# Kernel tuning notes

Measured on AMD Instinct MI355X. Metric: run time of the kernel, lower is better.

## Reference

```python
import jax, jax.numpy as jnp
import numpy as np

N_LAYERS = 5
EMB = 300
G = 2048
L_SEM = 10
V_SEM = 30
NUM_TASKS = 128
TAU = 1.0
GUM_TAU = 1.0
BN_EPS = 1e-5


def _bn(x, g, b):
    # training-mode batch norm (biased variance over batch dim)
    m = jnp.mean(x, 0)
    v = jnp.var(x, 0)
    return (x - m) / jnp.sqrt(v + BN_EPS) * g + b


def setup_inputs() -> dict:
    key = jax.random.key(0)
    ks = iter(jax.random.split(key, 64))
    N, E = 100000, 400000
    s = 0.02
    inp = {}
    inp['x_idx'] = jax.random.randint(next(ks), (N,), 0, 119)
    inp['edge_index'] = jax.random.randint(next(ks), (2, E), 0, N)
    inp['edge_attr'] = jax.random.randint(next(ks), (E,), 0, 5)
    inp['batch'] = jnp.sort(jax.random.randint(next(ks), (N,), 0, G))
    u = jax.random.uniform(next(ks), (G, L_SEM, V_SEM), minval=1e-8, maxval=1.0)
    inp['gumbel'] = -jnp.log(-jnp.log(u))  # standard Gumbel(0,1) noise
    nrm = lambda shape: jax.random.normal(next(ks), shape, dtype=jnp.float32) * s
    inp['atom_emb'] = nrm((119, EMB))
    inp['bond_emb'] = nrm((N_LAYERS, 5, EMB))
    inp['eps'] = jnp.zeros((N_LAYERS,), jnp.float32)
    inp['gin_W1'] = nrm((N_LAYERS, EMB, 2 * EMB)); inp['gin_b1'] = jnp.zeros((N_LAYERS, 2 * EMB))
    inp['gin_bn1_g'] = jnp.ones((N_LAYERS, 2 * EMB)); inp['gin_bn1_b'] = jnp.zeros((N_LAYERS, 2 * EMB))
    inp['gin_W2'] = nrm((N_LAYERS, 2 * EMB, EMB)); inp['gin_b2'] = jnp.zeros((N_LAYERS, EMB))
    inp['node_bn_g'] = jnp.ones((N_LAYERS, EMB)); inp['node_bn_b'] = jnp.zeros((N_LAYERS, EMB))
    M = N_LAYERS - 1
    inp['vn_W1'] = nrm((M, EMB, 2 * EMB)); inp['vn_b1'] = jnp.zeros((M, 2 * EMB))
    inp['vn_bn1_g'] = jnp.ones((M, 2 * EMB)); inp['vn_bn1_b'] = jnp.zeros((M, 2 * EMB))
    inp['vn_W2'] = nrm((M, 2 * EMB, EMB)); inp['vn_b2'] = jnp.zeros((M, EMB))
    inp['vn_bn2_g'] = jnp.ones((M, EMB)); inp['vn_bn2_b'] = jnp.zeros((M, EMB))
    inp['pre_W'] = nrm((EMB, L_SEM * V_SEM)); inp['pre_b'] = jnp.zeros((L_SEM * V_SEM,))
    inp['sel_W'] = nrm((V_SEM, 3)); inp['sel_b'] = jnp.zeros((3,))
    inp['aft_W'] = nrm((3 * L_SEM, EMB)); inp['aft_b'] = jnp.zeros((EMB,))
    inp['hW1'] = nrm((EMB, 128)); inp['hb1'] = jnp.zeros((128,))
    inp['hW2'] = nrm((128, 128)); inp['hb2'] = jnp.zeros((128,))
    inp['hW3'] = nrm((128, NUM_TASKS)); inp['hb3'] = jnp.zeros((NUM_TASKS,))
    return inp


def reference(x_idx, edge_index, edge_attr, batch, gumbel,
              atom_emb, bond_emb, eps,
              gin_W1, gin_b1, gin_bn1_g, gin_bn1_b, gin_W2, gin_b2,
              node_bn_g, node_bn_b,
              vn_W1, vn_b1, vn_bn1_g, vn_bn1_b, vn_W2, vn_b2, vn_bn2_g, vn_bn2_b,
              pre_W, pre_b, sel_W, sel_b, aft_W, aft_b,
              hW1, hb1, hW2, hb2, hW3, hb3):
    N = x_idx.shape[0]
    src, dst = edge_index[0], edge_index[1]
    h = atom_emb[x_idx]                               # [N, EMB]
    vn = jnp.zeros((G, EMB), h.dtype)                 # virtual node starts at zero embedding
    for l in range(N_LAYERS):
        hl = h + vn[batch]
        # GINConv: aggregate relu(x_src + bond_emb) onto dst, then MLP((1+eps)x + aggr)
        msg = jax.nn.relu(hl[src] + bond_emb[l][edge_attr])   # [E, EMB]
        agg = jax.ops.segment_sum(msg, dst, num_segments=N)
        t = (1.0 + eps[l]) * hl + agg
        t = jax.nn.relu(_bn(t @ gin_W1[l] + gin_b1[l], gin_bn1_g[l], gin_bn1_b[l]))
        t = t @ gin_W2[l] + gin_b2[l]
        t = _bn(t, node_bn_g[l], node_bn_b[l])
        if l < N_LAYERS - 1:
            t = jax.nn.relu(t)
            # virtual node update (dropout omitted: eval mode)
            vtmp = jax.ops.segment_sum(hl, batch, num_segments=G) + vn
            v1 = jax.nn.relu(_bn(vtmp @ vn_W1[l] + vn_b1[l], vn_bn1_g[l], vn_bn1_b[l]))
            vn = jax.nn.relu(_bn(v1 @ vn_W2[l] + vn_b2[l], vn_bn2_g[l], vn_bn2_b[l]))
        h = t
    # global mean pool
    cnt = jnp.maximum(jax.ops.segment_sum(jnp.ones((N,), h.dtype), batch, num_segments=G), 1.0)
    h_graph = jax.ops.segment_sum(h, batch, num_segments=G) / cnt[:, None]
    # SEM head: gumbel-softmax (hard, straight-through)
    logits = ((h_graph @ pre_W + pre_b) / TAU).reshape(G, L_SEM, V_SEM)
    y = (logits + gumbel) / GUM_TAU
    y_soft = jax.nn.softmax(y, axis=-1)
    y_hard = jax.nn.one_hot(jnp.argmax(y, axis=-1), V_SEM, dtype=y_soft.dtype)
    oht = jax.lax.stop_gradient(y_hard - y_soft) + y_soft
    msg_w = oht @ sel_W + sel_b                        # [G, L, 3]
    dis = msg_w.reshape(G, 3 * L_SEM) @ aft_W + aft_b  # [G, EMB]
    o = jax.nn.relu(dis @ hW1 + hb1)
    o = jax.nn.relu(o @ hW2 + hb2)
    return o @ hW3 + hb3                               # [G, num_tasks]
```

## Files before the change

### kernel.cpp

```cpp
#include <hip/hip_runtime.h>
#include <cstdint>

#define EMBD 300
#define GNUM 2048
#define LSEM 10
#define VSEM 30
#define NLAY 5
#define GRAM_KB 24

typedef __attribute__((ext_vector_type(8))) short short8v;
typedef __attribute__((ext_vector_type(4))) float f32x4;

__device__ __forceinline__ void split3(float x, short& h1, short& h2, short& h3) {
  unsigned u = __float_as_uint(x);
  unsigned uh = (u + 0x7FFFu + ((u >> 16) & 1u)) & 0xFFFF0000u;
  h1 = (short)(uh >> 16);
  float r = x - __uint_as_float(uh);
  unsigned v = __float_as_uint(r);
  unsigned vh = (v + 0x7FFFu + ((v >> 16) & 1u)) & 0xFFFF0000u;
  h2 = (short)(vh >> 16);
  float r2 = r - __uint_as_float(vh);
  unsigned w = __float_as_uint(r2);
  unsigned wh = (w + 0x7FFFu + ((w >> 16) & 1u)) & 0xFFFF0000u;
  h3 = (short)(wh >> 16);
}

__device__ __forceinline__ unsigned cvt_pk_bf16(float lo, float hi) {
  unsigned r;
  asm("v_cvt_pk_bf16_f32 %0, %1, %2" : "=v"(r) : "v"(lo), "v"(hi));
  return r;
}

__device__ __forceinline__ void split3_pair(float x0, float x1,
                                            unsigned& u1, unsigned& u2, unsigned& u3) {
  u1 = cvt_pk_bf16(x0, x1);
  float r0 = x0 - __uint_as_float(u1 << 16);
  float r1 = x1 - __uint_as_float(u1 & 0xFFFF0000u);
  u2 = cvt_pk_bf16(r0, r1);
  float s0 = r0 - __uint_as_float(u2 << 16);
  float s1 = r1 - __uint_as_float(u2 & 0xFFFF0000u);
  u3 = cvt_pk_bf16(s0, s1);
}

__global__ void k_diag(float* __restrict__ p, int n, float v) {
  int i = blockIdx.x * blockDim.x + threadIdx.x;
  if (i < n) p[i] = v;
}

__global__ void k_zero(float* __restrict__ p, int n) {
  int i = blockIdx.x * blockDim.x + threadIdx.x;
  if (i < n) p[i] = 0.f;
}

__global__ void k_seti(int* __restrict__ p, int n, int v) {
  int i = blockIdx.x * blockDim.x + threadIdx.x;
  if (i < n) p[i] = v;
}

__global__ void k_offsets(const int* __restrict__ batch, int N, int* __restrict__ off) {
  int g = blockIdx.x * blockDim.x + threadIdx.x;
  if (g > GNUM) return;
  int lo = 0, hi = N;
  while (lo < hi) { int mid = (lo + hi) >> 1; if (batch[mid] < g) lo = mid + 1; else hi = mid; }
  off[g] = lo;
}

__global__ void k_deg(const int* __restrict__ dst, int E, int* __restrict__ deg) {
  int e = blockIdx.x * blockDim.x + threadIdx.x;
  if (e < E) atomicAdd(&deg[dst[e]], 1);
}

__global__ void k_scan1(const int* __restrict__ deg, int N,
                        int* __restrict__ incl, int* __restrict__ part) {
  __shared__ int s[256];
  int tid = threadIdx.x;
  int i = blockIdx.x * 256 + tid;
  int v = (i < N) ? deg[i] : 0;
  s[tid] = v; __syncthreads();
  for (int o = 1; o < 256; o <<= 1) {
    int t = (tid >= o) ? s[tid - o] : 0;
    __syncthreads();
    s[tid] += t;
    __syncthreads();
  }
  if (i < N) incl[i] = s[tid];
  if (tid == 255) part[blockIdx.x] = s[255];
}

__global__ void k_scan2(int* __restrict__ part, int nb) {
  __shared__ int s[512];
  int t = threadIdx.x;
  if (nb <= 512) {
    int v = (t < nb) ? part[t] : 0;
    s[t] = v; __syncthreads();
    for (int o = 1; o < 512; o <<= 1) {
      int u = (t >= o) ? s[t - o] : 0;
      __syncthreads();
      s[t] += u;
      __syncthreads();
    }
    if (t < nb) part[t] = s[t] - v;
  } else if (t == 0) {
    int run = 0;
    for (int i = 0; i < nb; i++) { int x = part[i]; part[i] = run; run += x; }
  }
}

__global__ void k_scan3(const int* __restrict__ deg, const int* __restrict__ incl,
                        const int* __restrict__ part, int N, int E, int* __restrict__ off2) {
  int i = blockIdx.x * blockDim.x + threadIdx.x;
  if (i < N) off2[i] = part[i >> 8] + incl[i] - deg[i];
  if (i == 0) off2[N] = E;
}

__global__ void k_copyi(const int* __restrict__ a, int* __restrict__ b, int n) {
  int i = blockIdx.x * blockDim.x + threadIdx.x;
  if (i < n) b[i] = a[i];
}

__global__ void k_fill(const int* __restrict__ dst, int E,
                       int* __restrict__ cur, int* __restrict__ eix) {
  int e = blockIdx.x * blockDim.x + threadIdx.x;
  if (e >= E) return;
  int p = atomicAdd(&cur[dst[e]], 1);
  eix[p] = e;
}

template<bool FIRST>
__global__ void k_hl(const float* __restrict__ aemb, const int* __restrict__ x_idx,
                     const float* __restrict__ scale, const float* __restrict__ shift,
                     const int* __restrict__ batch, const float* __restrict__ vn,
                     const float* __restrict__ epsArr, int l,
                     float* pt, float* __restrict__ hl, int N)
{
  int i = blockIdx.x;
  int c = threadIdx.x;
  if (c >= EMBD) return;
  float x;
  if (FIRST) {
    x = aemb[(size_t)x_idx[i] * EMBD + c];
  } else {
    x = pt[(size_t)i * EMBD + c];
    x = fmaxf(fmaf(x, scale[c], shift[c]), 0.f);
  }
  float h = x + vn[(size_t)batch[i] * EMBD + c];
  hl[(size_t)i * EMBD + c] = h;
  pt[(size_t)i * EMBD + c] = (1.f + epsArr[l]) * h;
}

__global__ void k_gather(const int* __restrict__ off2, const int* __restrict__ eix,
                         const int* __restrict__ src, const int* __restrict__ eattr,
                         const float* __restrict__ hl, const float* __restrict__ bond,
                         float* __restrict__ tacc, int N)
{
  int node = blockIdx.x * 4 + (threadIdx.x >> 6);
  int lane = threadIdx.x & 63;
  if (node >= N) return;
  int p0 = off2[node], p1 = off2[node + 1];
  if (p0 == p1) return;
  float acc[5] = {0.f, 0.f, 0.f, 0.f, 0.f};
  for (int p = p0; p < p1; p++) {
    int e = eix[p];
    int s = src[e], a = eattr[e];
    const float* hr = hl + (size_t)s * EMBD;
    const float* br = bond + (size_t)a * EMBD;
    #pragma unroll
    for (int q = 0; q < 5; q++) {
      int c = lane + q * 64;
      if (c < EMBD) {
        float v = hr[c] + br[c];
        acc[q] += fmaxf(v, 0.f);
      }
    }
  }
  float* tr = tacc + (size_t)node * EMBD;
  #pragma unroll
  for (int q = 0; q < 5; q++) {
    int c = lane + q * 64;
    if (c < EMBD) tr[c] += acc[q];
  }
}

__global__ void k_splitW(const float* __restrict__ W, int K, int Kpad, int M,
                         short* __restrict__ planes)
{
  int idx = blockIdx.x * 256 + threadIdx.x;
  if (idx >= M * Kpad) return;
  int m = idx / Kpad, k = idx - m * Kpad;
  float x = (k < K) ? W[(size_t)k * M + m] : 0.f;
  short h1, h2, h3; split3(x, h1, h2, h3);
  size_t ps = (size_t)M * Kpad;
  planes[idx] = h1; planes[ps + idx] = h2; planes[2 * ps + idx] = h3;
}

template<int CT, bool AFUSE>
__global__ __launch_bounds__(256) void k_mgemm(
    const float* __restrict__ A, const short* __restrict__ Wp,
    const float* __restrict__ bias, float* __restrict__ C,
    int n, int K, int Kpad, int M,
    const float* __restrict__ ascale, const float* __restrict__ ashift)
{
  __shared__ __align__(16) short lsA[3][64][40];
  __shared__ __align__(16) short lsB[3][CT * 64][40];
  int tid = threadIdx.x;
  int row0 = blockIdx.x * 64;
  int col0 = blockIdx.y * (CT * 64);
  int l = tid & 63, wid = tid >> 6;
  int wr = wid >> 1, wc = wid & 1;
  int lr = l & 15, kb = (l >> 4) * 8, rbase = (l >> 4) * 4;
  int sar = tid >> 2;
  int sak = (tid & 3) * 8;
  size_t planeSz = (size_t)M * Kpad;

  f32x4 acc[2][CT * 2];
  #pragma unroll
  for (int i = 0; i < 2; i++)
    #pragma unroll
    for (int j = 0; j < CT * 2; j++) acc[i][j] = (f32x4){0.f, 0.f, 0.f, 0.f};

  for (int k0 = 0; k0 < Kpad; k0 += 32) {
    {
      int gr = row0 + sar;
      int kbase = k0 + sak;
      float x[8];
      if (gr < n && kbase + 7 < K) {
        const float* ap = A + (size_t)gr * K + kbase;
        float4 u0 = *reinterpret_cast<const float4*>(ap);
        float4 u1 = *reinterpret_cast<const float4*>(ap + 4);
        x[0] = u0.x; x[1] = u0.y; x[2] = u0.z; x[3] = u0.w;
        x[4] = u1.x; x[5] = u1.y; x[6] = u1.z; x[7] = u1.w;
        if (AFUSE) {
          float4 sc0 = *reinterpret_cast<const float4*>(ascale + kbase);
          float4 sc1 = *reinterpret_cast<const float4*>(ascale + kbase + 4);
          float4 sf0 = *reinterpret_cast<const float4*>(ashift + kbase);
          float4 sf1 = *reinterpret_cast<const float4*>(ashift + kbase + 4);
          x[0] = fmaxf(fmaf(x[0], sc0.x, sf0.x), 0.f);
          x[1] = fmaxf(fmaf(x[1], sc0.y, sf0.y), 0.f);
          x[2] = fmaxf(fmaf(x[2], sc0.z, sf0.z), 0.f);
          x[3] = fmaxf(fmaf(x[3], sc0.w, sf0.w), 0.f);
          x[4] = fmaxf(fmaf(x[4], sc1.x, sf1.x), 0.f);
          x[5] = fmaxf(fmaf(x[5], sc1.y, sf1.y), 0.f);
          x[6] = fmaxf(fmaf(x[6], sc1.z, sf1.z), 0.f);
          x[7] = fmaxf(fmaf(x[7], sc1.w, sf1.w), 0.f);
        }
      } else {
        #pragma unroll
        for (int j = 0; j < 8; j++) {
          int k = kbase + j;
          float v = 0.f;
          if (gr < n && k < K) {
            v = A[(size_t)gr * K + k];
            if (AFUSE) v = fmaxf(fmaf(v, ascale[k], ashift[k]), 0.f);
          }
          x[j] = v;
        }
      }
      uint4 q1, q2, q3;
      unsigned* p1 = (unsigned*)&q1; unsigned* p2 = (unsigned*)&q2; unsigned* p3 = (unsigned*)&q3;
      #pragma unroll
      for (int j = 0; j < 4; j++) split3_pair(x[2 * j], x[2 * j + 1], p1[j], p2[j], p3[j]);
      *reinterpret_cast<uint4*>(&lsA[0][sar][sak]) = q1;
      *reinterpret_cast<uint4*>(&lsA[1][sar][sak]) = q2;
      *reinterpret_cast<uint4*>(&lsA[2][sar][sak]) = q3;
    }
    if constexpr (CT == 2) {
      int sbc = tid >> 1;
      int sbk = (tid & 1) * 16;
      int gc = col0 + sbc;
      #pragma unroll
      for (int p = 0; p < 3; p++) {
        short8v v0, v1;
        if (gc < M) {
          const short* bp = Wp + (size_t)p * planeSz + (size_t)gc * Kpad + k0 + sbk;
          v0 = *reinterpret_cast<const short8v*>(bp);
          v1 = *reinterpret_cast<const short8v*>(bp + 8);
        } else {
          #pragma unroll
          for (int j = 0; j < 8; j++) { v0[j] = 0; v1[j] = 0; }
        }
        *reinterpret_cast<short8v*>(&lsB[p][sbc][sbk]) = v0;
        *reinterpret_cast<short8v*>(&lsB[p][sbc][sbk + 8]) = v1;
      }
    } else {
      int sbc = tid >> 2;
      int sbk = (tid & 3) * 8;
      int gc = col0 + sbc;
      #pragma unroll
      for (int p = 0; p < 3; p++) {
        short8v v0;
        if (gc < M) {
          const short* bp = Wp + (size_t)p * planeSz + (size_t)gc * Kpad + k0 + sbk;
          v0 = *reinterpret_cast<const short8v*>(bp);
        } else {
          #pragma unroll
          for (int j = 0; j < 8; j++) v0[j] = 0;
        }
        *reinterpret_cast<short8v*>(&lsB[p][sbc][sbk]) = v0;
      }
    }
    __syncthreads();
    short8v fa[3][2];
    #pragma unroll
    for (int p = 0; p < 3; p++)
      #pragma unroll
      for (int rf = 0; rf < 2; rf++)
        fa[p][rf] = *reinterpret_cast<const short8v*>(&lsA[p][wr * 32 + rf * 16 + lr][kb]);
    #pragma unroll
    for (int cf = 0; cf < CT * 2; cf++) {
      int bcol = wc * (CT * 32) + cf * 16 + lr;
      short8v fb0 = *reinterpret_cast<const short8v*>(&lsB[0][bcol][kb]);
      short8v fb1 = *reinterpret_cast<const short8v*>(&lsB[1][bcol][kb]);
      short8v fb2 = *reinterpret_cast<const short8v*>(&lsB[2][bcol][kb]);
      #pragma unroll
      for (int rf = 0; rf < 2; rf++) {
        f32x4 a = acc[rf][cf];
        a = __builtin_amdgcn_mfma_f32_16x16x32_bf16(fa[0][rf], fb0, a, 0, 0, 0);
        a = __builtin_amdgcn_mfma_f32_16x16x32_bf16(fa[0][rf], fb1, a, 0, 0, 0);
        a = __builtin_amdgcn_mfma_f32_16x16x32_bf16(fa[1][rf], fb0, a, 0, 0, 0);
        a = __builtin_amdgcn_mfma_f32_16x16x32_bf16(fa[1][rf], fb1, a, 0, 0, 0);
        a = __builtin_amdgcn_mfma_f32_16x16x32_bf16(fa[0][rf], fb2, a, 0, 0, 0);
        a = __builtin_amdgcn_mfma_f32_16x16x32_bf16(fa[2][rf], fb0, a, 0, 0, 0);
        acc[rf][cf] = a;
      }
    }
    __syncthreads();
  }
  #pragma unroll
  for (int rf = 0; rf < 2; rf++) {
    #pragma unroll
    for (int cf = 0; cf < CT * 2; cf++) {
      int col = col0 + wc * (CT * 32) + cf * 16 + lr;
      if (col >= M) continue;
      float bv = bias[col];
      #pragma unroll
      for (int r = 0; r < 4; r++) {
        int row = row0 + wr * 32 + rf * 16 + rbase + r;
        if (row < n) C[(size_t)row * M + col] = acc[rf][cf][r] + bv;
      }
    }
  }
}

template<bool AFUSE, bool ORELU>
__global__ __launch_bounds__(256) void k_gemm(
    const float* __restrict__ A, const float* __restrict__ W,
    const float* __restrict__ bias, float* __restrict__ C,
    int N, int K, int M,
    const float* __restrict__ ascale, const float* __restrict__ ashift)
{
  __shared__ __align__(16) float As[16][72];
  __shared__ __align__(16) float Bs[16][72];
  int tid = threadIdx.x;
  int row0 = blockIdx.x * 64;
  int col0 = blockIdx.y * 64;
  int tx = tid & 15, ty = tid >> 4;
  bool kvec = ((K & 3) == 0);
  bool mvec = ((M & 3) == 0);
  float acc[4][4] = {};
  for (int k0 = 0; k0 < K; k0 += 16) {
    {
      int r = tid >> 2;
      int kq = (tid & 3) * 4;
      int gr = row0 + r;
      float a0 = 0.f, a1 = 0.f, a2 = 0.f, a3 = 0.f;
      if (gr < N) {
        const float* ap = A + (size_t)gr * K + k0 + kq;
        int k = k0 + kq;
        if (kvec && k + 3 < K) {
          float4 t = *reinterpret_cast<const float4*>(ap);
          a0 = t.x; a1 = t.y; a2 = t.z; a3 = t.w;
        } else {
          if (k + 0 < K) a0 = ap[0];
          if (k + 1 < K) a1 = ap[1];
          if (k + 2 < K) a2 = ap[2];
          if (k + 3 < K) a3 = ap[3];
        }
        if (AFUSE) {
          if (k + 0 < K) a0 = fmaxf(fmaf(a0, ascale[k + 0], ashift[k + 0]), 0.f);
          if (k + 1 < K) a1 = fmaxf(fmaf(a1, ascale[k + 1], ashift[k + 1]), 0.f);
          if (k + 2 < K) a2 = fmaxf(fmaf(a2, ascale[k + 2], ashift[k + 2]), 0.f);
          if (k + 3 < K) a3 = fmaxf(fmaf(a3, ascale[k + 3], ashift[k + 3]), 0.f);
        }
      }
      As[kq + 0][r] = a0; As[kq + 1][r] = a1; As[kq + 2][r] = a2; As[kq + 3][r] = a3;
    }
    {
      int kk = tid >> 4;
      int j = (tid & 15) * 4;
      int gk = k0 + kk;
      float4 bv = {0.f, 0.f, 0.f, 0.f};
      if (gk < K) {
        const float* wp = W + (size_t)gk * M + col0 + j;
        if (mvec && col0 + j + 3 < M) {
          bv = *reinterpret_cast<const float4*>(wp);
        } else {
          if (col0 + j + 0 < M) bv.x = wp[0];
          if (col0 + j + 1 < M) bv.y = wp[1];
          if (col0 + j + 2 < M) bv.z = wp[2];
          if (col0 + j + 3 < M) bv.w = wp[3];
        }
      }
      *reinterpret_cast<float4*>(&Bs[kk][j]) = bv;
    }
    __syncthreads();
    #pragma unroll
    for (int kk = 0; kk < 16; kk++) {
      float4 a4 = *reinterpret_cast<const float4*>(&As[kk][ty * 4]);
      float4 b4 = *reinterpret_cast<const float4*>(&Bs[kk][tx * 4]);
      float a[4] = {a4.x, a4.y, a4.z, a4.w};
      float b[4] = {b4.x, b4.y, b4.z, b4.w};
      #pragma unroll
      for (int u = 0; u < 4; u++)
        #pragma unroll
        for (int v = 0; v < 4; v++)
          acc[u][v] = fmaf(a[u], b[v], acc[u][v]);
    }
    __syncthreads();
  }
  float bv[4];
  #pragma unroll
  for (int v = 0; v < 4; v++) { int gc = col0 + tx * 4 + v; bv[v] = (gc < M) ? bias[gc] : 0.f; }
  #pragma unroll
  for (int u = 0; u < 4; u++) {
    int gr = row0 + ty * 4 + u;
    if (gr >= N) continue;
    int gc0 = col0 + tx * 4;
    float val[4];
    #pragma unroll
    for (int v = 0; v < 4; v++) {
      float x = acc[u][v] + bv[v];
      if (ORELU) x = fmaxf(x, 0.f);
      val[v] = x;
    }
    if (mvec && gc0 + 3 < M) {
      float4 o = {val[0], val[1], val[2], val[3]};
      *reinterpret_cast<float4*>(C + (size_t)gr * M + gc0) = o;
    } else {
      #pragma unroll
      for (int v = 0; v < 4; v++) {
        int gc = gc0 + v;
        if (gc < M) C[(size_t)gr * M + gc] = val[v];
      }
    }
  }
}

__global__ __launch_bounds__(256) void k_gram(const float* __restrict__ A, int N,
                                              double* __restrict__ gpart)
{
  int bx = blockIdx.x;
  int ti = 0;
  {
    const int o1 = 5, o2 = 9, o3 = 12, o4 = 14;
    if (bx >= o1) ti = 1;
    if (bx >= o2) ti = 2;
    if (bx >= o3) ti = 3;
    if (bx >= o4) ti = 4;
  }
  const int offs[5] = {0, 5, 9, 12, 14};
  int tj = ti + (bx - offs[ti]);
  int I = ti * 64, J = tj * 64;
  __shared__ __align__(16) float LI[128][68];
  __shared__ __align__(16) float LJ[128][68];
  int tid = threadIdx.x;
  int tx = tid & 15, ty = tid >> 4;
  double dacc[4][4] = {};
  for (int rb = blockIdx.y; rb * 128 < N; rb += gridDim.y) {
    int r0 = rb * 128;
    {
      int rbase = tid >> 4;
      int c4 = (tid & 15) * 4;
      #pragma unroll
      for (int s = 0; s < 8; s++) {
        int r = rbase + s * 16;
        int gr = r0 + r;
        float4 vi = {0.f, 0.f, 0.f, 0.f}, vj = {0.f, 0.f, 0.f, 0.f};
        if (gr < N) {
          int ci = I + c4;
          if (ci + 3 < EMBD) vi = *reinterpret_cast<const float4*>(A + (size_t)gr * EMBD + ci);
          int cj = J + c4;
          if (cj + 3 < EMBD) vj = *reinterpret_cast<const float4*>(A + (size_t)gr * EMBD + cj);
        }
        *reinterpret_cast<float4*>(&LI[r][c4]) = vi;
        *reinterpret_cast<float4*>(&LJ[r][c4]) = vj;
      }
    }
    __syncthreads();
    float facc[4][4] = {};
    #pragma unroll 2
    for (int k = 0; k < 128; k++) {
      float4 a4 = *reinterpret_cast<const float4*>(&LI[k][ty * 4]);
      float4 b4 = *reinterpret_cast<const float4*>(&LJ[k][tx * 4]);
      float a[4] = {a4.x, a4.y, a4.z, a4.w};
      float b[4] = {b4.x, b4.y, b4.z, b4.w};
      #pragma unroll
      for (int u = 0; u < 4; u++)
        #pragma unroll
        for (int v = 0; v < 4; v++)
          facc[u][v] = fmaf(a[u], b[v], facc[u][v]);
    }
    #pragma unroll
    for (int u = 0; u < 4; u++)
      #pragma unroll
      for (int v = 0; v < 4; v++)
        dacc[u][v] += (double)facc[u][v];
    __syncthreads();
  }
  size_t base = ((size_t)blockIdx.y * 15 + bx) * 4096;
  #pragma unroll
  for (int u = 0; u < 4; u++)
    #pragma unroll
    for (int v = 0; v < 4; v++)
      gpart[base + (size_t)(ty * 4 + u) * 64 + tx * 4 + v] = dacc[u][v];
}

__global__ void k_gramfin(const double* __restrict__ gpart, double* __restrict__ G)
{
  int e = blockIdx.x * 256 + threadIdx.x;
  if (e >= 15 * 4096) return;
  int tile = e >> 12;
  int ii = (e >> 6) & 63, jj = e & 63;
  const int tit[15] = {0,0,0,0,0,1,1,1,1,2,2,2,3,3,4};
  const int tjt[15] = {0,1,2,3,4,1,2,3,4,2,3,4,3,4,4};
  int gi = tit[tile] * 64 + ii, gj = tjt[tile] * 64 + jj;
  if (gi >= EMBD || gj >= EMBD) return;
  double s = 0.0;
  for (int kb = 0; kb < GRAM_KB; kb++)
    s += gpart[((size_t)kb * 15 + tile) * 4096 + ii * 64 + jj];
  G[(size_t)gi * EMBD + gj] = s;
  G[(size_t)gj * EMBD + gi] = s;
}

__global__ void k_bn1gram(const double* __restrict__ G, const double* __restrict__ cbuf,
                          const float* __restrict__ W1, const float* __restrict__ b1,
                          const float* __restrict__ g, const float* __restrict__ b,
                          int n, float* __restrict__ sc, float* __restrict__ sh)
{
  int j = blockIdx.x;
  int t = threadIdx.x;
  __shared__ double ws[EMBD];
  __shared__ double red[256];
  for (int k = t; k < EMBD; k += 256) ws[k] = (double)W1[(size_t)k * 600 + j];
  __syncthreads();
  int i1 = 256 + t;
  double y0 = 0.0, y1 = 0.0;
  for (int k = 0; k < EMBD; k++) {
    double wk = ws[k];
    y0 += G[(size_t)k * EMBD + t] * wk;
    if (i1 < EMBD) y1 += G[(size_t)k * EMBD + i1] * wk;
  }
  double part = ws[t] * y0 + ((i1 < EMBD) ? ws[i1] * y1 : 0.0);
  double dpart = cbuf[t] * ws[t] + ((i1 < EMBD) ? cbuf[i1] * ws[i1] : 0.0);
  red[t] = part; __syncthreads();
  for (int w = 128; w > 0; w >>= 1) { if (t < w) red[t] += red[t + w]; __syncthreads(); }
  double Q = red[0]; __syncthreads();
  red[t] = dpart; __syncthreads();
  for (int w = 128; w > 0; w >>= 1) { if (t < w) red[t] += red[t + w]; __syncthreads(); }
  if (t == 0) {
    double d = red[0];
    double bj = (double)b1[j];
    double S = d + (double)n * bj;
    double Qf = Q + 2.0 * bj * d + (double)n * bj * bj;
    double m = S / n;
    double var = Qf / n - m * m;
    double inv = 1.0 / sqrt(var + 1e-5);
    double scv = (double)g[j] * inv;
    sc[j] = (float)scv;
    sh[j] = (float)((double)b[j] - m * scv);
  }
}

__global__ void k_colstats(const float* __restrict__ X, int n, int C,
                           double* __restrict__ psum, double* __restrict__ psq)
{
  int tid = threadIdx.x;
  int col = blockIdx.x * 64 + (tid & 63);
  int rl = tid >> 6;
  double s = 0.0, q = 0.0;
  if (col < C) {
    int stride = gridDim.y * 4;
    for (int r = blockIdx.y * 4 + rl; r < n; r += stride) {
      double x = (double)X[(size_t)r * C + col];
      s += x; q += x * x;
    }
  }
  __shared__ double ls[2][4][64];
  ls[0][rl][tid & 63] = s;
  ls[1][rl][tid & 63] = q;
  __syncthreads();
  if (rl == 0 && col < C) {
    int c = tid & 63;
    double S = ls[0][0][c] + ls[0][1][c] + ls[0][2][c] + ls[0][3][c];
    double Q = ls[1][0][c] + ls[1][1][c] + ls[1][2][c] + ls[1][3][c];
    psum[(size_t)blockIdx.y * C + col] = S;
    psq [(size_t)blockIdx.y * C + col] = Q;
  }
}

__global__ void k_redcol(const double* __restrict__ psum, int R, int C, double* __restrict__ cbuf)
{
  int c = blockIdx.x * blockDim.x + threadIdx.x;
  if (c >= C) return;
  double s = 0.0;
  for (int r = 0; r < R; r++) s += psum[(size_t)r * C + c];
  cbuf[c] = s;
}

__global__ void k_finstats(const double* __restrict__ psum, const double* __restrict__ psq,
                           int R, int M, int n,
                           const float* __restrict__ g, const float* __restrict__ b,
                           float* __restrict__ sc, float* __restrict__ sh)
{
  int j = blockIdx.x;
  int t = threadIdx.x;
  double s = 0.0, q = 0.0;
  for (int r = t; r < R; r += 256) { s += psum[(size_t)r * M + j]; q += psq[(size_t)r * M + j]; }
  __shared__ double ls[256], lq[256];
  ls[t] = s; lq[t] = q; __syncthreads();
  for (int w = 128; w > 0; w >>= 1) {
    if (t < w) { ls[t] += ls[t + w]; lq[t] += lq[t + w]; }
    __syncthreads();
  }
  if (t == 0) {
    double m = ls[0] / n;
    double v = lq[0] / n - m * m;
    double inv = 1.0 / sqrt(v + 1e-5);
    double scv = (double)g[j] * inv;
    sc[j] = (float)scv;
    sh[j] = (float)((double)b[j] - m * scv);
  }
}

__global__ void k_vnseg(const float* __restrict__ hl, const int* __restrict__ off,
                        const float* __restrict__ vn, float* __restrict__ vtmp)
{
  int g = blockIdx.x;
  int c = threadIdx.x;
  if (c >= EMBD) return;
  int r0 = off[g], r1 = off[g + 1];
  float s = 0.f;
  for (int r = r0; r < r1; r++) s += hl[(size_t)r * EMBD + c];
  vtmp[(size_t)g * EMBD + c] = s + vn[(size_t)g * EMBD + c];
}

__global__ void k_vnfinal(const float* __restrict__ vnraw, const float* __restrict__ scale,
                          const float* __restrict__ shift, float* __restrict__ vn, int total)
{
  int i = blockIdx.x * blockDim.x + threadIdx.x;
  if (i >= total) return;
  int c = i % EMBD;
  vn[i] = fmaxf(fmaf(vnraw[i], scale[c], shift[c]), 0.f);
}

__global__ void k_pool(const float* __restrict__ t2, const int* __restrict__ off,
                       const float* __restrict__ scale, const float* __restrict__ shift,
                       float* __restrict__ hg)
{
  int g = blockIdx.x;
  int c = threadIdx.x;
  if (c >= EMBD) return;
  int r0 = off[g], r1 = off[g + 1];
  float s = 0.f;
  for (int r = r0; r < r1; r++) s += t2[(size_t)r * EMBD + c];
  int cnt = r1 - r0;
  float denom = (cnt > 0) ? (float)cnt : 1.f;
  hg[(size_t)g * EMBD + c] = (scale[c] * s + shift[c] * (float)cnt) / denom;
}

__global__ void k_sem(const float* __restrict__ logits, const float* __restrict__ gum,
                      const float* __restrict__ selW, const float* __restrict__ selb,
                      float* __restrict__ msgw)
{
  int idx = blockIdx.x * blockDim.x + threadIdx.x;
  if (idx >= GNUM * LSEM) return;
  int g = idx / LSEM, l = idx % LSEM;
  const float* lp = logits + (size_t)g * (LSEM * VSEM) + l * VSEM;
  const float* gp = gum + (size_t)g * (LSEM * VSEM) + l * VSEM;
  float best = -1e30f; int bi = 0;
  for (int v = 0; v < VSEM; v++) {
    float y = lp[v] + gp[v];
    if (y > best) { best = y; bi = v; }
  }
  float* o = msgw + (size_t)g * (3 * LSEM) + l * 3;
  o[0] = selW[bi * 3 + 0] + selb[0];
  o[1] = selW[bi * 3 + 1] + selb[1];
  o[2] = selW[bi * 3 + 2] + selb[2];
}

template<bool AFUSE, bool ORELU>
static void gemm(const float* A, const float* W, const float* b, float* C,
                 int n, int k, int m, const float* sc, const float* sh, hipStream_t st)
{
  dim3 grid((n + 63) / 64, (m + 63) / 64);
  k_gemm<AFUSE, ORELU><<<grid, 256, 0, st>>>(A, W, b, C, n, k, m, sc, sh);
}

extern "C" void kernel_launch(void* const* d_in, const int* in_sizes, int n_in,
                              void* d_out, int out_size, void* d_ws, size_t ws_size,
                              hipStream_t stream)
{
  const int*   x_idx     = (const int*)d_in[0];
  const int*   eidx      = (const int*)d_in[1];
  const int*   eattr     = (const int*)d_in[2];
  const int*   batch     = (const int*)d_in[3];
  const float* gumbel    = (const float*)d_in[4];
  const float* atom_emb  = (const float*)d_in[5];
  const float* bond_emb  = (const float*)d_in[6];
  const float* eps       = (const float*)d_in[7];
  const float* gin_W1    = (const float*)d_in[8];
  const float* gin_b1    = (const float*)d_in[9];
  const float* gin_bn1_g = (const float*)d_in[10];
  const float* gin_bn1_b = (const float*)d_in[11];
  const float* gin_W2    = (const float*)d_in[12];
  const float* gin_b2    = (const float*)d_in[13];
  const float* node_bn_g = (const float*)d_in[14];
  const float* node_bn_b = (const float*)d_in[15];
  const float* vn_W1     = (const float*)d_in[16];
  const float* vn_b1     = (const float*)d_in[17];
  const float* vn_bn1_g  = (const float*)d_in[18];
  const float* vn_bn1_b  = (const float*)d_in[19];
  const float* vn_W2     = (const float*)d_in[20];
  const float* vn_b2     = (const float*)d_in[21];
  const float* vn_bn2_g  = (const float*)d_in[22];
  const float* vn_bn2_b  = (const float*)d_in[23];
  const float* pre_W     = (const float*)d_in[24];
  const float* pre_b     = (const float*)d_in[25];
  const float* sel_W     = (const float*)d_in[26];
  const float* sel_b     = (const float*)d_in[27];
  const float* aft_W     = (const float*)d_in[28];
  const float* aft_b     = (const float*)d_in[29];
  const float* hW1       = (const float*)d_in[30];
  const float* hb1       = (const float*)d_in[31];
  const float* hW2       = (const float*)d_in[32];
  const float* hb2       = (const float*)d_in[33];
  const float* hW3       = (const float*)d_in[34];
  const float* hb3       = (const float*)d_in[35];

  const int N = in_sizes[0];
  const int E = in_sizes[2];
  const int RB = 128;
  float* out = (float*)d_out;
  (void)n_in;

  char* ws = (char*)d_ws;
  size_t pos = 0;
  auto alloc = [&](size_t bytes) -> char* {
    char* p = ws + pos;
    pos = (pos + bytes + 255) & ~(size_t)255;
    return p;
  };
  int*    off   = (int*)   alloc((GNUM + 1) * sizeof(int));
  float*  hbuf0 = (float*) alloc((size_t)N * EMBD * 4);
  float*  hbuf1 = (float*) alloc((size_t)N * EMBD * 4);
  double* psum  = (double*)alloc((size_t)RB * 600 * 8);
  double* psq   = (double*)alloc((size_t)RB * 600 * 8);
  float*  vn    = (float*) alloc((size_t)GNUM * EMBD * 4);
  float*  vtmp  = (float*) alloc((size_t)GNUM * EMBD * 4);
  float*  vnraw = (float*) alloc((size_t)GNUM * EMBD * 4);
  double* cbuf  = (double*)alloc(EMBD * 8);
  int*    off2  = (int*)   alloc((size_t)(N + 1) * 4);
  int*    eix   = (int*)   alloc((size_t)E * 4);
  short*  wsplit1 = (short*)alloc((size_t)600 * 320 * 3 * 2);
  short*  wsplit2 = (short*)alloc((size_t)300 * 608 * 3 * 2);
  float*  s1    = (float*) alloc(600 * 4);
  float*  sh1   = (float*) alloc(600 * 4);
  float*  s2    = (float*) alloc(EMBD * 4);
  float*  sh2   = (float*) alloc(EMBD * 4);
  float*  vs1   = (float*) alloc(600 * 4);
  float*  vsh1  = (float*) alloc(600 * 4);
  float*  vs2   = (float*) alloc(EMBD * 4);
  float*  vsh2  = (float*) alloc(EMBD * 4);

  const size_t gpartBytes = (size_t)GRAM_KB * 15 * 4096 * 8;
  const size_t gBytes     = (size_t)EMBD * EMBD * 8;
  const size_t csrScratch = (size_t)N * 4 * 3 + 4096;
  const long long CH_MIN  = 2048;
  size_t slack = 1u << 20;
  size_t region_need = gpartBytes + gBytes;
  if (region_need < csrScratch) region_need = csrScratch;
  size_t t1_min = (size_t)CH_MIN * 600 * 4;
  if (region_need < t1_min) region_need = t1_min;

  if (ws_size < pos + region_need + slack) {
    float v = 1000.f + (float)(ws_size >> 20);
    k_diag<<<(out_size + 255) / 256, 256, 0, stream>>>(out, out_size, v);
    return;
  }

  size_t regionBytes = ws_size - pos - slack;
  char* region = ws + pos;
  int* deg  = (int*)region;
  int* incl = (int*)(region + (size_t)N * 4);
  int* cur  = (int*)(region + (size_t)N * 8);
  int* part = (int*)(region + (size_t)N * 12);
  double* gpart = (double*)region;
  double* G     = (double*)(region + gpartBytes);
  float*  t1buf = (float*)region;
  int CH;
  {
    long long ch = (long long)(regionBytes / (600ull * 4ull));
    if (ch > 32768) ch = 32768;
    ch &= ~63LL;
    if (ch < CH_MIN) ch = CH_MIN;
    long long npad = ((long long)N + 63) & ~63LL;
    if (ch > npad && npad >= CH_MIN) ch = npad;
    CH = (int)ch;
  }
  float* v1 = t1buf;
  float* hg     = vnraw;
  float* logits = t1buf;
  float* msgw   = t1buf + (size_t)GNUM * EMBD;
  float* dis    = vtmp;
  float* o1     = vn;
  float* o2     = vn + (size_t)GNUM * 128;

  k_zero<<<(GNUM * EMBD + 255) / 256, 256, 0, stream>>>(vn, GNUM * EMBD);
  k_offsets<<<(GNUM + 1 + 255) / 256, 256, 0, stream>>>(batch, N, off);

  const int* esrc = eidx;
  const int* edst = eidx + E;

  {
    int NB = (N + 255) / 256;
    k_seti<<<(N + 255) / 256, 256, 0, stream>>>(deg, N, 0);
    k_deg<<<(E + 255) / 256, 256, 0, stream>>>(edst, E, deg);
    k_scan1<<<NB, 256, 0, stream>>>(deg, N, incl, part);
    k_scan2<<<1, 512, 0, stream>>>(part, NB);
    k_scan3<<<(N + 255) / 256, 256, 0, stream>>>(deg, incl, part, N, E, off2);
    k_copyi<<<(N + 255) / 256, 256, 0, stream>>>(off2, cur, N);
    k_fill<<<(E + 255) / 256, 256, 0, stream>>>(edst, E, cur, eix);
  }

  float* hb[2] = {hbuf0, hbuf1};

  for (int l = 0; l < NLAY; l++) {
    float* tac = hb[l & 1];
    float* hlb = hb[(l + 1) & 1];

    if (l == 0)
      k_hl<true><<<N, 320, 0, stream>>>(atom_emb, x_idx, nullptr, nullptr, batch, vn, eps, l, tac, hlb, N);
    else
      k_hl<false><<<N, 320, 0, stream>>>(nullptr, nullptr, s2, sh2, batch, vn, eps, l, tac, hlb, N);

    k_gather<<<(N + 3) / 4, 256, 0, stream>>>(off2, eix, esrc, eattr, hlb,
                                              bond_emb + (size_t)l * 5 * EMBD, tac, N);

    if (l < NLAY - 1)
      k_vnseg<<<GNUM, 320, 0, stream>>>(hlb, off, vn, vtmp);

    k_colstats<<<dim3(5, RB), 256, 0, stream>>>(tac, N, EMBD, psum, psq);
    k_redcol<<<2, 256, 0, stream>>>(psum, RB, EMBD, cbuf);
    k_gram<<<dim3(15, GRAM_KB), 256, 0, stream>>>(tac, N, gpart);
    k_gramfin<<<240, 256, 0, stream>>>(gpart, G);
    k_bn1gram<<<600, 256, 0, stream>>>(G, cbuf, gin_W1 + (size_t)l * EMBD * 600,
                                       gin_b1 + (size_t)l * 600,
                                       gin_bn1_g + (size_t)l * 600, gin_bn1_b + (size_t)l * 600,
                                       N, s1, sh1);

    k_splitW<<<(600 * 320 + 255) / 256, 256, 0, stream>>>(gin_W1 + (size_t)l * EMBD * 600, 300, 320, 600, wsplit1);
    k_splitW<<<(300 * 608 + 255) / 256, 256, 0, stream>>>(gin_W2 + (size_t)l * 600 * EMBD, 600, 608, 300, wsplit2);

    for (int r0 = 0; r0 < N; r0 += CH) {
      int nr = (N - r0 < CH) ? (N - r0) : CH;
      dim3 g1((nr + 63) / 64, 5);
      k_mgemm<2, false><<<g1, 256, 0, stream>>>(tac + (size_t)r0 * EMBD, wsplit1,
                                                gin_b1 + (size_t)l * 600, t1buf,
                                                nr, 300, 320, 600, nullptr, nullptr);
      dim3 g2((nr + 63) / 64, 5);
      k_mgemm<1, true><<<g2, 256, 0, stream>>>(t1buf, wsplit2,
                                               gin_b2 + (size_t)l * EMBD, hlb + (size_t)r0 * EMBD,
                                               nr, 600, 608, 300, s1, sh1);
    }
    k_colstats<<<dim3(5, RB), 256, 0, stream>>>(hlb, N, EMBD, psum, psq);
    k_finstats<<<EMBD, 256, 0, stream>>>(psum, psq, RB, EMBD, N,
                                         node_bn_g + (size_t)l * EMBD, node_bn_b + (size_t)l * EMBD, s2, sh2);

    if (l < NLAY - 1) {
      gemm<false, false>(vtmp, vn_W1 + (size_t)l * EMBD * 600, vn_b1 + (size_t)l * 600, v1,
                         GNUM, EMBD, 600, nullptr, nullptr, stream);
      k_colstats<<<dim3(10, RB), 256, 0, stream>>>(v1, GNUM, 600, psum, psq);
      k_finstats<<<600, 256, 0, stream>>>(psum, psq, RB, 600, GNUM,
                                          vn_bn1_g + (size_t)l * 600, vn_bn1_b + (size_t)l * 600, vs1, vsh1);
      gemm<true, false>(v1, vn_W2 + (size_t)l * 600 * EMBD, vn_b2 + (size_t)l * EMBD, vnraw,
                        GNUM, 600, EMBD, vs1, vsh1, stream);
      k_colstats<<<dim3(5, RB), 256, 0, stream>>>(vnraw, GNUM, EMBD, psum, psq);
      k_finstats<<<EMBD, 256, 0, stream>>>(psum, psq, RB, EMBD, GNUM,
                                           vn_bn2_g + (size_t)l * EMBD, vn_bn2_b + (size_t)l * EMBD, vs2, vsh2);
      k_vnfinal<<<(GNUM * EMBD + 255) / 256, 256, 0, stream>>>(vnraw, vs2, vsh2, vn, GNUM * EMBD);
    }
  }

  float* lastH = hb[NLAY & 1];
  k_pool<<<GNUM, 320, 0, stream>>>(lastH, off, s2, sh2, hg);

  gemm<false, false>(hg, pre_W, pre_b, logits, GNUM, EMBD, LSEM * VSEM, nullptr, nullptr, stream);
  k_sem<<<(GNUM * LSEM + 255) / 256, 256, 0, stream>>>(logits, gumbel, sel_W, sel_b, msgw);
  gemm<false, false>(msgw, aft_W, aft_b, dis, GNUM, 3 * LSEM, EMBD, nullptr, nullptr, stream);
  gemm<false, true>(dis, hW1, hb1, o1, GNUM, EMBD, 128, nullptr, nullptr, stream);
  gemm<false, true>(o1, hW2, hb2, o2, GNUM, 128, 128, nullptr, nullptr, stream);
  gemm<false, false>(o2, hW3, hb3, out, GNUM, 128, 128, nullptr, nullptr, stream);
}
```

Before: 10.42 ms.

## Compute Gram matrix with split-bf16 MFMA instead of scalar FP32 FMAs

Replaces the FP32 FMA Gram kernel (used for the BN1 statistics shortcut) with an MFMA version. Each float is split into three bf16 parts and six bf16 MFMA products are accumulated to approximate FP32 precision. This moves the N×300×300 Gram work onto the matrix units, which should cut the ALU cost. In exchange, accumulation is now FP32 across all rows of a block's slice, where the old kernel flushed partials into FP64 every 128 rows, so rounding error may grow.

```diff
diff --git a/kernel.cpp b/kernel.cpp
--- a/kernel.cpp
+++ b/kernel.cpp
@@ -341,6 +341,117 @@
   }
 }
 
+__global__ __launch_bounds__(256) void k_mgram(const float* __restrict__ A, int N,
+                                               double* __restrict__ gpart)
+{
+  int bx = blockIdx.x;
+  int ti = 0;
+  {
+    const int o1 = 5, o2 = 9, o3 = 12, o4 = 14;
+    if (bx >= o1) ti = 1;
+    if (bx >= o2) ti = 2;
+    if (bx >= o3) ti = 3;
+    if (bx >= o4) ti = 4;
+  }
+  const int offs[5] = {0, 5, 9, 12, 14};
+  int tj = ti + (bx - offs[ti]);
+  int I = ti * 64, J = tj * 64;
+  __shared__ __align__(16) short lsI[3][64][40];
+  __shared__ __align__(16) short lsJ[3][64][40];
+  int tid = threadIdx.x;
+  int l = tid & 63, wid = tid >> 6;
+  int wr = wid >> 1, wc = wid & 1;
+  int lr = l & 15, kb = (l >> 4) * 8, rbase = (l >> 4) * 4;
+  int sr = tid & 31;
+  int sc0 = (tid >> 5) * 8;
+
+  f32x4 acc[2][2];
+  #pragma unroll
+  for (int i = 0; i < 2; i++)
+    #pragma unroll
+    for (int j = 0; j < 2; j++) acc[i][j] = (f32x4){0.f, 0.f, 0.f, 0.f};
+
+  for (int r0 = blockIdx.y * 32; r0 < N; r0 += gridDim.y * 32) {
+    int gr = r0 + sr;
+    float xi[8], xj[8];
+    {
+      int ci = I + sc0;
+      if (gr < N && ci + 7 < EMBD) {
+        const float* ap = A + (size_t)gr * EMBD + ci;
+        float4 u0 = *reinterpret_cast<const float4*>(ap);
+        float4 u1 = *reinterpret_cast<const float4*>(ap + 4);
+        xi[0] = u0.x; xi[1] = u0.y; xi[2] = u0.z; xi[3] = u0.w;
+        xi[4] = u1.x; xi[5] = u1.y; xi[6] = u1.z; xi[7] = u1.w;
+      } else {
+        #pragma unroll
+        for (int j = 0; j < 8; j++) {
+          int c = ci + j;
+          xi[j] = (gr < N && c < EMBD) ? A[(size_t)gr * EMBD + c] : 0.f;
+        }
+      }
+      int cj = J + sc0;
+      if (gr < N && cj + 7 < EMBD) {
+        const float* ap = A + (size_t)gr * EMBD + cj;
+        float4 u0 = *reinterpret_cast<const float4*>(ap);
+        float4 u1 = *reinterpret_cast<const float4*>(ap + 4);
+        xj[0] = u0.x; xj[1] = u0.y; xj[2] = u0.z; xj[3] = u0.w;
+        xj[4] = u1.x; xj[5] = u1.y; xj[6] = u1.z; xj[7] = u1.w;
+      } else {
+        #pragma unroll
+        for (int j = 0; j < 8; j++) {
+          int c = cj + j;
+          xj[j] = (gr < N && c < EMBD) ? A[(size_t)gr * EMBD + c] : 0.f;
+        }
+      }
+    }
+    #pragma unroll
+    for (int j = 0; j < 8; j++) {
+      short a1, a2, a3; split3(xi[j], a1, a2, a3);
+      lsI[0][sc0 + j][sr] = a1; lsI[1][sc0 + j][sr] = a2; lsI[2][sc0 + j][sr] = a3;
+      short b1, b2, b3; split3(xj[j], b1, b2, b3);
+      lsJ[0][sc0 + j][sr] = b1; lsJ[1][sc0 + j][sr] = b2; lsJ[2][sc0 + j][sr] = b3;
+    }
+    __syncthreads();
+    short8v fa[3][2];
+    #pragma unroll
+    for (int p = 0; p < 3; p++)
+      #pragma unroll
+      for (int rf = 0; rf < 2; rf++)
+        fa[p][rf] = *reinterpret_cast<const short8v*>(&lsI[p][wr * 32 + rf * 16 + lr][kb]);
+    #pragma unroll
+    for (int cf = 0; cf < 2; cf++) {
+      int bcol = wc * 32 + cf * 16 + lr;
+      short8v fb0 = *reinterpret_cast<const short8v*>(&lsJ[0][bcol][kb]);
+      short8v fb1 = *reinterpret_cast<const short8v*>(&lsJ[1][bcol][kb]);
+      short8v fb2 = *reinterpret_cast<const short8v*>(&lsJ[2][bcol][kb]);
+      #pragma unroll
+      for (int rf = 0; rf < 2; rf++) {
+        f32x4 a = acc[rf][cf];
+        a = __builtin_amdgcn_mfma_f32_16x16x32_bf16(fa[0][rf], fb0, a, 0, 0, 0);
+        a = __builtin_amdgcn_mfma_f32_16x16x32_bf16(fa[0][rf], fb1, a, 0, 0, 0);
+        a = __builtin_amdgcn_mfma_f32_16x16x32_bf16(fa[1][rf], fb0, a, 0, 0, 0);
+        a = __builtin_amdgcn_mfma_f32_16x16x32_bf16(fa[1][rf], fb1, a, 0, 0, 0);
+        a = __builtin_amdgcn_mfma_f32_16x16x32_bf16(fa[0][rf], fb2, a, 0, 0, 0);
+        a = __builtin_amdgcn_mfma_f32_16x16x32_bf16(fa[2][rf], fb0, a, 0, 0, 0);
+        acc[rf][cf] = a;
+      }
+    }
+    __syncthreads();
+  }
+  size_t base = ((size_t)blockIdx.y * 15 + bx) * 4096;
+  #pragma unroll
+  for (int rf = 0; rf < 2; rf++)
+    #pragma unroll
+    for (int cf = 0; cf < 2; cf++) {
+      int col = wc * 32 + cf * 16 + lr;
+      #pragma unroll
+      for (int r = 0; r < 4; r++) {
+        int row = wr * 32 + rf * 16 + rbase + r;
+        gpart[base + (size_t)row * 64 + col] = (double)acc[rf][cf][r];
+      }
+    }
+}
+
 template<bool AFUSE, bool ORELU>
 __global__ __launch_bounds__(256) void k_gemm(
     const float* __restrict__ A, const float* __restrict__ W,
@@ -443,75 +554,6 @@
       }
     }
   }
-}
-
-__global__ __launch_bounds__(256) void k_gram(const float* __restrict__ A, int N,
-                                              double* __restrict__ gpart)
-{
-  int bx = blockIdx.x;
-  int ti = 0;
-  {
-    const int o1 = 5, o2 = 9, o3 = 12, o4 = 14;
-    if (bx >= o1) ti = 1;
-    if (bx >= o2) ti = 2;
-    if (bx >= o3) ti = 3;
-    if (bx >= o4) ti = 4;
-  }
-  const int offs[5] = {0, 5, 9, 12, 14};
-  int tj = ti + (bx - offs[ti]);
-  int I = ti * 64, J = tj * 64;
-  __shared__ __align__(16) float LI[128][68];
-  __shared__ __align__(16) float LJ[128][68];
-  int tid = threadIdx.x;
-  int tx = tid & 15, ty = tid >> 4;
-  double dacc[4][4] = {};
-  for (int rb = blockIdx.y; rb * 128 < N; rb += gridDim.y) {
-    int r0 = rb * 128;
-    {
-      int rbase = tid >> 4;
-      int c4 = (tid & 15) * 4;
-      #pragma unroll
-      for (int s = 0; s < 8; s++) {
-        int r = rbase + s * 16;
-        int gr = r0 + r;
-        float4 vi = {0.f, 0.f, 0.f, 0.f}, vj = {0.f, 0.f, 0.f, 0.f};
-        if (gr < N) {
-          int ci = I + c4;
-          if (ci + 3 < EMBD) vi = *reinterpret_cast<const float4*>(A + (size_t)gr * EMBD + ci);
-          int cj = J + c4;
-          if (cj + 3 < EMBD) vj = *reinterpret_cast<const float4*>(A + (size_t)gr * EMBD + cj);
-        }
-        *reinterpret_cast<float4*>(&LI[r][c4]) = vi;
-        *reinterpret_cast<float4*>(&LJ[r][c4]) = vj;
-      }
-    }
-    __syncthreads();
-    float facc[4][4] = {};
-    #pragma unroll 2
-    for (int k = 0; k < 128; k++) {
-      float4 a4 = *reinterpret_cast<const float4*>(&LI[k][ty * 4]);
-      float4 b4 = *reinterpret_cast<const float4*>(&LJ[k][tx * 4]);
-      float a[4] = {a4.x, a4.y, a4.z, a4.w};
-      float b[4] = {b4.x, b4.y, b4.z, b4.w};
-      #pragma unroll
-      for (int u = 0; u < 4; u++)
-        #pragma unroll
-        for (int v = 0; v < 4; v++)
-          facc[u][v] = fmaf(a[u], b[v], facc[u][v]);
-    }
-    #pragma unroll
-    for (int u = 0; u < 4; u++)
-      #pragma unroll
-      for (int v = 0; v < 4; v++)
-        dacc[u][v] += (double)facc[u][v];
-    __syncthreads();
-  }
-  size_t base = ((size_t)blockIdx.y * 15 + bx) * 4096;
-  #pragma unroll
-  for (int u = 0; u < 4; u++)
-    #pragma unroll
-    for (int v = 0; v < 4; v++)
-      gpart[base + (size_t)(ty * 4 + u) * 64 + tx * 4 + v] = dacc[u][v];
 }
 
 __global__ void k_gramfin(const double* __restrict__ gpart, double* __restrict__ G)
@@ -850,7 +892,7 @@
 
     k_colstats<<<dim3(5, RB), 256, 0, stream>>>(tac, N, EMBD, psum, psq);
     k_redcol<<<2, 256, 0, stream>>>(psum, RB, EMBD, cbuf);
-    k_gram<<<dim3(15, GRAM_KB), 256, 0, stream>>>(tac, N, gpart);
+    k_mgram<<<dim3(15, GRAM_KB), 256, 0, stream>>>(tac, N, gpart);
     k_gramfin<<<240, 256, 0, stream>>>(gpart, G);
     k_bn1gram<<<600, 256, 0, stream>>>(G, cbuf, gin_W1 + (size_t)l * EMBD * 600,
                                        gin_b1 + (size_t)l * 600,
```

After: 9.888 ms. -5.1%, faster.
